# Kernel optimization log

Measured on AMD Instinct MI355X. Metric: run time of the kernel, lower is better.

Reference implementation:

```python
import jax, jax.numpy as jnp
import numpy as np


def setup_inputs() -> dict:
    key = jax.random.key(0)
    kx, kw, kb = jax.random.split(key, 3)
    x = jax.random.normal(kx, (4, 2048, 4096), dtype=jnp.float32)
    weight = jax.random.normal(kw, (4096, 4096), dtype=jnp.float32) * 0.02
    bias = jax.random.normal(kb, (4096,), dtype=jnp.float32) * 0.02
    return {"x": x, "weight": weight, "bias": bias}


def _binarize_except_outliers(w):
    # Outlier mask from global weight stats (computed from w itself; in torch it
    # is cached after the first call but the values are identical every step).
    mean = jnp.mean(w)
    std = jnp.std(w, ddof=1)  # torch.std default is the unbiased estimator
    lower = mean - 1.96 * std
    upper = mean + 1.96 * std
    outliers = (w < lower) | (w > upper)
    keep = (~outliers).astype(w.dtype)
    # scaling_factor in the torch code: w[~outliers].abs().mean(-1) on the
    # flattened masked-select -> a single SCALAR, detached from the graph.
    scale = jax.lax.stop_gradient(jnp.sum(jnp.abs(w) * keep) / jnp.sum(keep))
    # NOTE: the torch code assigns STE-sign values and then immediately
    # overwrites them with w * scale, so the effective math is:
    w_bin = jnp.where(outliers, w, w * scale)
    return w_bin


def reference(x, weight, bias):
    w_bin = _binarize_except_outliers(weight)  # [out, in]
    # F.linear(x, w, b) = x @ w.T + b
    return jnp.einsum("bsi,oi->bso", x, w_bin) + bias
```

## Files before the change

kernel.cpp:

```cpp
#include <hip/hip_runtime.h>
#include <hip/hip_bf16.h>
#include <math.h>

#define MDIM 8192
#define NDIM 4096
#define KDIM 4096
#define WELEMS 16777216
#define XELEMS 33554432

typedef __attribute__((ext_vector_type(8))) short bf16x8;
typedef __attribute__((ext_vector_type(4))) float f32x4;

__device__ __forceinline__ unsigned short f2bf(float f) {
  unsigned int u = __float_as_uint(f);
  u += 0x7fffu + ((u >> 16) & 1u);
  return (unsigned short)(u >> 16);
}

__device__ __forceinline__ void gload16(const void* g, void* l) {
  __builtin_amdgcn_global_load_lds(
      (const __attribute__((address_space(1))) void*)g,
      (__attribute__((address_space(3))) void*)l, 16, 0, 0);
}

template <int MODE>
__global__ __launch_bounds__(256)
void np_stage1(const float* __restrict__ w, float* __restrict__ C,
               float* __restrict__ C2, const float* __restrict__ scal) {
  __shared__ float ls[32], ls2[32];
  const int t = threadIdx.x;
  const int leaf = t >> 3, j = t & 7;
  const size_t base = (size_t)blockIdx.x * 4096 + leaf * 128 + j;
  float mean = 0.f, lower = 0.f, upper = 0.f;
  if (MODE == 1) mean = scal[0];
  if (MODE == 2) { lower = scal[1]; upper = scal[2]; }
  float r = 0.f, r2 = 0.f;
#pragma unroll
  for (int s = 0; s < 16; s++) {
    float v = w[base + s * 8];
    float tv, tv2 = 0.f;
    if (MODE == 0) tv = v;
    else if (MODE == 1) { float x = v - mean; tv = __fmul_rn(x, x); }
    else {
      bool keep = !(v < lower || v > upper);
      tv = keep ? fabsf(v) : 0.f;
      tv2 = keep ? 1.f : 0.f;
    }
    if (s == 0) { r = tv; r2 = tv2; } else { r += tv; r2 += tv2; }
  }
  r += __shfl_xor(r, 1); r += __shfl_xor(r, 2); r += __shfl_xor(r, 4);
  if (MODE == 2) { r2 += __shfl_xor(r2, 1); r2 += __shfl_xor(r2, 2); r2 += __shfl_xor(r2, 4); }
  if (j == 0) { ls[leaf] = r; if (MODE == 2) ls2[leaf] = r2; }
  __syncthreads();
  if (t == 0) {
    float tmp[32];
    for (int i = 0; i < 32; i++) tmp[i] = ls[i];
    for (int n = 32; n > 1; n >>= 1)
      for (int i = 0; i < n / 2; i++) tmp[i] = tmp[2 * i] + tmp[2 * i + 1];
    C[blockIdx.x] = tmp[0];
    if (MODE == 2) {
      for (int i = 0; i < 32; i++) tmp[i] = ls2[i];
      for (int n = 32; n > 1; n >>= 1)
        for (int i = 0; i < n / 2; i++) tmp[i] = tmp[2 * i] + tmp[2 * i + 1];
      C2[blockIdx.x] = tmp[0];
    }
  }
}

template <int MODE>
__global__ __launch_bounds__(256)
void np_stage2(const float* __restrict__ C, const float* __restrict__ C2,
               float* __restrict__ scal) {
  __shared__ float ls[256], ls2[256];
  const int t = threadIdx.x;
  {
    float v[16];
    for (int i = 0; i < 16; i++) v[i] = C[t * 16 + i];
    for (int n = 16; n > 1; n >>= 1)
      for (int i = 0; i < n / 2; i++) v[i] = v[2 * i] + v[2 * i + 1];
    ls[t] = v[0];
    if (MODE == 2) {
      for (int i = 0; i < 16; i++) v[i] = C2[t * 16 + i];
      for (int n = 16; n > 1; n >>= 1)
        for (int i = 0; i < n / 2; i++) v[i] = v[2 * i] + v[2 * i + 1];
      ls2[t] = v[0];
    }
  }
  __syncthreads();
  if (t == 0) {
    float tmp[256];
    for (int i = 0; i < 256; i++) tmp[i] = ls[i];
    for (int n = 256; n > 1; n >>= 1)
      for (int i = 0; i < n / 2; i++) tmp[i] = tmp[2 * i] + tmp[2 * i + 1];
    float S = tmp[0];
    if (MODE == 0) {
      scal[0] = S / 16777216.0f;
    } else if (MODE == 1) {
      float var = S / 16777215.0f;
      float sd = sqrtf(var);
      float mean = scal[0];
      scal[1] = mean - __fmul_rn(1.96f, sd);
      scal[2] = mean + __fmul_rn(1.96f, sd);
    } else {
      for (int i = 0; i < 256; i++) tmp[i] = ls2[i];
      for (int n = 256; n > 1; n >>= 1)
        for (int i = 0; i < n / 2; i++) tmp[i] = tmp[2 * i] + tmp[2 * i + 1];
      scal[3] = S / tmp[0];
    }
  }
}

__device__ __forceinline__ void pack8(const float* __restrict__ p, unsigned short* dst,
                                      bool dobin, float lower, float upper, float scale) {
  float4 u = *(const float4*)p;
  float4 v = *(const float4*)(p + 4);
  float f[8] = {u.x, u.y, u.z, u.w, v.x, v.y, v.z, v.w};
  unsigned int r[4];
#pragma unroll
  for (int j = 0; j < 4; j++) {
    float a = f[2 * j], b = f[2 * j + 1];
    if (dobin) {
      bool oa = (a < lower) || (a > upper);
      bool ob = (b < lower) || (b > upper);
      a = oa ? a : __fmul_rn(a, scale);
      b = ob ? b : __fmul_rn(b, scale);
    }
    r[j] = (unsigned int)f2bf(a) | ((unsigned int)f2bf(b) << 16);
  }
  *(uint4*)dst = make_uint4(r[0], r[1], r[2], r[3]);
}

__global__ __launch_bounds__(256)
void convert_w(const float* __restrict__ w, unsigned short* __restrict__ wb,
               const float* __restrict__ scal) {
  float lower = scal[1], upper = scal[2], scale = scal[3];
  int tid = blockIdx.x * blockDim.x + threadIdx.x;
  int nth = gridDim.x * blockDim.x;
  int nc = WELEMS / 8;
  for (int i = tid; i < nc; i += nth)
    pack8(w + (size_t)i * 8, wb + (size_t)i * 8, true, lower, upper, scale);
}

__global__ __launch_bounds__(256)
void convert_x(const float* __restrict__ x, unsigned short* __restrict__ xb) {
  int tid = blockIdx.x * blockDim.x + threadIdx.x;
  int nth = gridDim.x * blockDim.x;
  int nc = XELEMS / 8;
  for (int i = tid; i < nc; i += nth)
    pack8(x + (size_t)i * 8, xb + (size_t)i * 8, false, 0.f, 0.f, 0.f);
}


#define VM2  asm volatile("s_waitcnt vmcnt(2)" ::: "memory")
#define VM0  asm volatile("s_waitcnt vmcnt(0)" ::: "memory")
#define LGK8 asm volatile("s_waitcnt lgkmcnt(8)" ::: "memory")
#define PSYNC { asm volatile("" ::: "memory"); __builtin_amdgcn_s_barrier(); asm volatile("" ::: "memory"); }

#define LDA(buf, mh) { \
  a[0][0] = *(const bf16x8*)&sA[buf][wm][((mh)*64 +  0 + fr)*64 + koo0]; \
  a[0][1] = *(const bf16x8*)&sA[buf][wm][((mh)*64 +  0 + fr)*64 + koo1]; \
  a[1][0] = *(const bf16x8*)&sA[buf][wm][((mh)*64 + 16 + fr)*64 + koo0]; \
  a[1][1] = *(const bf16x8*)&sA[buf][wm][((mh)*64 + 16 + fr)*64 + koo1]; \
  a[2][0] = *(const bf16x8*)&sA[buf][wm][((mh)*64 + 32 + fr)*64 + koo0]; \
  a[2][1] = *(const bf16x8*)&sA[buf][wm][((mh)*64 + 32 + fr)*64 + koo1]; \
  a[3][0] = *(const bf16x8*)&sA[buf][wm][((mh)*64 + 48 + fr)*64 + koo0]; \
  a[3][1] = *(const bf16x8*)&sA[buf][wm][((mh)*64 + 48 + fr)*64 + koo1]; }

#define LDB(buf, nh) { \
  b[0][0] = *(const bf16x8*)&sB[buf][wnh][(wnq*64 + (nh)*32 +  0 + fr)*64 + koo0]; \
  b[0][1] = *(const bf16x8*)&sB[buf][wnh][(wnq*64 + (nh)*32 +  0 + fr)*64 + koo1]; \
  b[1][0] = *(const bf16x8*)&sB[buf][wnh][(wnq*64 + (nh)*32 + 16 + fr)*64 + koo0]; \
  b[1][1] = *(const bf16x8*)&sB[buf][wnh][(wnq*64 + (nh)*32 + 16 + fr)*64 + koo1]; }

#define MM1(m, n, ks) acc[m][n] = __builtin_amdgcn_mfma_f32_16x16x32_bf16(a[(m)&3][ks], b[(n)&1][ks], acc[m][n], 0, 0, 0)
#define MMKS(mh, nh, ks) { \
  MM1((mh)*4+0, (nh)*2+0, ks); MM1((mh)*4+0, (nh)*2+1, ks); \
  MM1((mh)*4+1, (nh)*2+0, ks); MM1((mh)*4+1, (nh)*2+1, ks); \
  MM1((mh)*4+2, (nh)*2+0, ks); MM1((mh)*4+2, (nh)*2+1, ks); \
  MM1((mh)*4+3, (nh)*2+0, ks); MM1((mh)*4+3, (nh)*2+1, ks); }
#define MM(mh, nh) { \
  __builtin_amdgcn_s_setprio(1); \
  MMKS(mh, nh, 0); MMKS(mh, nh, 1); \
  __builtin_amdgcn_s_setprio(0); }

#define STGA(buf, q, ku) { \
  gload16(xbp + aoff[0][q] + (ku), &sA[buf][0][(q)*4096 + t8]); \
  gload16(xbp + aoff[1][q] + (ku), &sA[buf][1][(q)*4096 + t8]); }
#define STGB(buf, h, ku) { \
  gload16(wbp + boff[h][0] + (ku), &sB[buf][h][t8]); \
  gload16(wbp + boff[h][1] + (ku), &sB[buf][h][4096 + t8]); }

__global__ __launch_bounds__(512, 2)
void gemm256(const unsigned short* __restrict__ xbp, const unsigned short* __restrict__ wbp,
             const float* __restrict__ bias, float* __restrict__ out) {
  __shared__ unsigned short sA[2][2][8192];
  __shared__ unsigned short sB[2][2][8192];

  const int bid = blockIdx.x;
  const int swz = (bid & 7) * 64 + (bid >> 3);
  const int bm = swz >> 4;
  const int bn = swz & 15;

  const int t = threadIdx.x;
  const int lane = t & 63;
  const int wid = t >> 6;
  const int wm = wid >> 2;
  const int wn = wid & 3;
  const int wnh = wn >> 1;
  const int wnq = wn & 1;
  const int fr = lane & 15;
  const int ko = (lane >> 4) * 8;
  const int xr = (fr & 7) << 3;
  const int koo0 = ko ^ xr;
  const int koo1 = (32 + ko) ^ xr;

  const int t8 = t * 8;
  const int rl = t >> 3;
  const int cs = ((t & 7) * 8) ^ ((rl & 7) << 3);
  size_t aoff[2][2], boff[2][2];
#pragma unroll
  for (int h = 0; h < 2; h++)
#pragma unroll
    for (int q = 0; q < 2; q++) {
      aoff[h][q] = (size_t)(bm * 256 + h * 128 + q * 64 + rl) * KDIM + cs;
      boff[h][q] = (size_t)(bn * 256 + h * 128 + q * 64 + rl) * KDIM + cs;
    }

  f32x4 acc[8][4];
#pragma unroll
  for (int i = 0; i < 8; i++)
#pragma unroll
    for (int j = 0; j < 4; j++) acc[i][j] = {0.f, 0.f, 0.f, 0.f};

  bf16x8 a[4][2], b[2][2];

  STGA(0, 0, 0); STGA(0, 1, 0); STGB(0, 0, 0); STGB(0, 1, 0);
  STGA(1, 0, 64);
  VM2; PSYNC;

  const int NIT = KDIM / 128;
  for (int it = 0; it < NIT; ++it) {
    const bool last = (it == NIT - 1);
    const int kuB = it * 128 + 64;
    const int kuN = kuB + 64;

    LDA(0, 0); LDB(0, 0);
    STGA(1, 1, kuB);
    LGK8; PSYNC;
    MM(0, 0); PSYNC;

    LDB(0, 1);
    STGB(1, 0, kuB);
    PSYNC;
    MM(0, 1); PSYNC;

    LDA(0, 1);
    STGB(1, 1, kuB);
    PSYNC;
    MM(1, 1); PSYNC;

    LDB(0, 0);
    if (!last) STGA(0, 0, kuN);
    if (last) { VM0; } else { VM2; }
    PSYNC;
    MM(1, 0); PSYNC;

    LDA(1, 0); LDB(1, 0);
    if (!last) STGA(0, 1, kuN);
    LGK8; PSYNC;
    MM(0, 0); PSYNC;

    LDB(1, 1);
    if (!last) STGB(0, 0, kuN);
    PSYNC;
    MM(0, 1); PSYNC;

    LDA(1, 1);
    if (!last) STGB(0, 1, kuN);
    PSYNC;
    MM(1, 1); PSYNC;

    LDB(1, 0);
    if (!last) {
      STGA(1, 0, kuN + 64);
      VM2;
    }
    PSYNC;
    MM(1, 0); PSYNC;
  }

#pragma unroll
  for (int nn = 0; nn < 4; ++nn) {
    const int col = bn * 256 + wn * 64 + nn * 16 + (lane & 15);
    const float bv = bias[col];
#pragma unroll
    for (int m = 0; m < 8; ++m) {
      const int row0 = bm * 256 + wm * 128 + m * 16 + (lane >> 4) * 4;
#pragma unroll
      for (int q = 0; q < 4; ++q)
        out[(size_t)(row0 + q) * NDIM + col] = acc[m][nn][q] + bv;
    }
  }
}

template <bool A_BF16, bool B_BF16>
__global__ __launch_bounds__(256)
void gemm_bt(const void* __restrict__ Av, const void* __restrict__ Bv,
             const float* __restrict__ bias, float* __restrict__ out,
             const float* __restrict__ scal) {
  __shared__ unsigned short sAt[2][128 * 32];
  __shared__ unsigned short sBt[2][128 * 32];
  float lower = 0.f, upper = 0.f, scale = 0.f;
  if constexpr (!B_BF16) { lower = scal[1]; upper = scal[2]; scale = scal[3]; }
  const unsigned short* Ab = (const unsigned short*)Av;
  const float* Af = (const float*)Av;
  const unsigned short* Bb = (const unsigned short*)Bv;
  const float* Bf = (const float*)Bv;
  int bid = blockIdx.x;
  int swz = (bid & 7) * 256 + (bid >> 3);
  int bm = swz >> 5, bn = swz & 31;
  const int t = threadIdx.x, lane = t & 63, wid = t >> 6;
  const int wm = wid >> 1, wn = wid & 1;
  const int e0 = t * 8, e1 = e0 + 2048;
  const size_t aOff0 = (size_t)(bm * 128 + (e0 >> 5)) * KDIM + (e0 & 31);
  const size_t aOff1 = (size_t)(bm * 128 + (e1 >> 5)) * KDIM + (e1 & 31);
  const size_t bOff0 = (size_t)(bn * 128 + (e0 >> 5)) * KDIM + (e0 & 31);
  const size_t bOff1 = (size_t)(bn * 128 + (e1 >> 5)) * KDIM + (e1 & 31);
  f32x4 acc[4][4];
#pragma unroll
  for (int i = 0; i < 4; i++)
#pragma unroll
    for (int j = 0; j < 4; j++) acc[i][j] = {0.f, 0.f, 0.f, 0.f};
  auto stage = [&](int buf, int k0) {
    if constexpr (A_BF16) {
      gload16(Ab + aOff0 + k0, &sAt[buf][e0]);
      gload16(Ab + aOff1 + k0, &sAt[buf][e1]);
    } else {
      pack8(Af + aOff0 + k0, &sAt[buf][e0], false, 0.f, 0.f, 0.f);
      pack8(Af + aOff1 + k0, &sAt[buf][e1], false, 0.f, 0.f, 0.f);
    }
    if constexpr (B_BF16) {
      gload16(Bb + bOff0 + k0, &sBt[buf][e0]);
      gload16(Bb + bOff1 + k0, &sBt[buf][e1]);
    } else {
      pack8(Bf + bOff0 + k0, &sBt[buf][e0], true, lower, upper, scale);
      pack8(Bf + bOff1 + k0, &sBt[buf][e1], true, lower, upper, scale);
    }
  };
  stage(0, 0);
  const int NT = KDIM / 32;
  const int ko = (lane >> 4) * 8, fr = lane & 15;
  for (int tt = 0; tt < NT; ++tt) {
    int cur = tt & 1;
    __syncthreads();
    if (tt + 1 < NT) stage(cur ^ 1, (tt + 1) * 32);
    bf16x8 a[4], b[4];
#pragma unroll
    for (int i = 0; i < 4; i++) {
      a[i] = *(const bf16x8*)&sAt[cur][(wm * 64 + i * 16 + fr) * 32 + ko];
      b[i] = *(const bf16x8*)&sBt[cur][(wn * 64 + i * 16 + fr) * 32 + ko];
    }
#pragma unroll
    for (int i = 0; i < 4; i++)
#pragma unroll
      for (int j = 0; j < 4; j++)
        acc[i][j] = __builtin_amdgcn_mfma_f32_16x16x32_bf16(a[i], b[j], acc[i][j], 0, 0, 0);
  }
  const int colbase = bn * 128 + wn * 64 + (lane & 15);
  const int rowbase = bm * 128 + wm * 64 + (lane >> 4) * 4;
#pragma unroll
  for (int j = 0; j < 4; j++) {
    int col = colbase + j * 16;
    float bv = bias[col];
#pragma unroll
    for (int i = 0; i < 4; i++) {
      int row0 = rowbase + i * 16;
#pragma unroll
      for (int q = 0; q < 4; q++)
        out[(size_t)(row0 + q) * NDIM + col] = acc[i][j][q] + bv;
    }
  }
}

extern "C" void kernel_launch(void* const* d_in, const int* in_sizes, int n_in,
                              void* d_out, int out_size, void* d_ws, size_t ws_size,
                              hipStream_t stream) {
  const float* x = (const float*)d_in[0];
  const float* w = (const float*)d_in[1];
  const float* bias = (const float*)d_in[2];
  float* out = (float*)d_out;
  char* ws = (char*)d_ws;

  const size_t xb_b = (size_t)XELEMS * 2;
  const size_t wb_b = (size_t)WELEMS * 2;
  const size_t c_b = 4 * 4096 * sizeof(float);
  const bool full = ws_size >= xb_b + wb_b + c_b + 64;
  const bool wonly = !full && ws_size >= wb_b + c_b + 64;

  unsigned short *xb = nullptr, *wb = nullptr;
  float *C1, *scal;
  if (full) {
    xb = (unsigned short*)ws;
    wb = (unsigned short*)(ws + xb_b);
    C1 = (float*)(ws + xb_b + wb_b);
  } else if (wonly) {
    wb = (unsigned short*)ws;
    C1 = (float*)(ws + wb_b);
  } else {
    C1 = (float*)ws;
  }
  float* C2 = C1 + 4096;
  float* C3 = C2 + 4096;
  float* C4 = C3 + 4096;
  scal = C4 + 4096;

  np_stage1<0><<<dim3(4096), dim3(256), 0, stream>>>(w, C1, nullptr, scal);
  np_stage2<0><<<dim3(1), dim3(256), 0, stream>>>(C1, nullptr, scal);
  np_stage1<1><<<dim3(4096), dim3(256), 0, stream>>>(w, C2, nullptr, scal);
  np_stage2<1><<<dim3(1), dim3(256), 0, stream>>>(C2, nullptr, scal);
  np_stage1<2><<<dim3(4096), dim3(256), 0, stream>>>(w, C3, C4, scal);
  np_stage2<2><<<dim3(1), dim3(256), 0, stream>>>(C3, C4, scal);

  if (full) {
    convert_w<<<dim3(2048), dim3(256), 0, stream>>>(w, wb, scal);
    convert_x<<<dim3(4096), dim3(256), 0, stream>>>(x, xb);
    gemm256<<<dim3(512), dim3(512), 0, stream>>>(xb, wb, bias, out);
  } else if (wonly) {
    convert_w<<<dim3(2048), dim3(256), 0, stream>>>(w, wb, scal);
    gemm_bt<false, true><<<dim3(2048), dim3(256), 0, stream>>>(x, wb, bias, out, scal);
  } else {
    gemm_bt<false, false><<<dim3(2048), dim3(256), 0, stream>>>(x, w, bias, out, scal);
  }
}
```

Baseline: 431.5 us.

## Keep both B fragment halves in registers and prefetch B tiles earlier

Splits the B register fragments into two sets (b0/b1) so the fourth MFMA phase reuses b0 instead of reloading it from LDS, removing one LDS read batch per half-iteration. The global-to-LDS schedule is reordered so B tiles for the next K-step are issued earlier, in larger groups, with the wait threshold raised from vmcnt(2) to vmcnt(6). This deepens prefetch of W relative to X. The cost is more VGPRs and possible hazards if the reordered loads overwrite LDS buffers still being read.

```diff
diff --git a/kernel.cpp b/kernel.cpp
--- a/kernel.cpp
+++ b/kernel.cpp
@@ -151,7 +151,7 @@
 }
 
 
-#define VM2  asm volatile("s_waitcnt vmcnt(2)" ::: "memory")
+#define VM6  asm volatile("s_waitcnt vmcnt(6)" ::: "memory")
 #define VM0  asm volatile("s_waitcnt vmcnt(0)" ::: "memory")
 #define LGK8 asm volatile("s_waitcnt lgkmcnt(8)" ::: "memory")
 #define PSYNC { asm volatile("" ::: "memory"); __builtin_amdgcn_s_barrier(); asm volatile("" ::: "memory"); }
@@ -166,21 +166,21 @@
   a[3][0] = *(const bf16x8*)&sA[buf][wm][((mh)*64 + 48 + fr)*64 + koo0]; \
   a[3][1] = *(const bf16x8*)&sA[buf][wm][((mh)*64 + 48 + fr)*64 + koo1]; }
 
-#define LDB(buf, nh) { \
-  b[0][0] = *(const bf16x8*)&sB[buf][wnh][(wnq*64 + (nh)*32 +  0 + fr)*64 + koo0]; \
-  b[0][1] = *(const bf16x8*)&sB[buf][wnh][(wnq*64 + (nh)*32 +  0 + fr)*64 + koo1]; \
-  b[1][0] = *(const bf16x8*)&sB[buf][wnh][(wnq*64 + (nh)*32 + 16 + fr)*64 + koo0]; \
-  b[1][1] = *(const bf16x8*)&sB[buf][wnh][(wnq*64 + (nh)*32 + 16 + fr)*64 + koo1]; }
-
-#define MM1(m, n, ks) acc[m][n] = __builtin_amdgcn_mfma_f32_16x16x32_bf16(a[(m)&3][ks], b[(n)&1][ks], acc[m][n], 0, 0, 0)
-#define MMKS(mh, nh, ks) { \
-  MM1((mh)*4+0, (nh)*2+0, ks); MM1((mh)*4+0, (nh)*2+1, ks); \
-  MM1((mh)*4+1, (nh)*2+0, ks); MM1((mh)*4+1, (nh)*2+1, ks); \
-  MM1((mh)*4+2, (nh)*2+0, ks); MM1((mh)*4+2, (nh)*2+1, ks); \
-  MM1((mh)*4+3, (nh)*2+0, ks); MM1((mh)*4+3, (nh)*2+1, ks); }
-#define MM(mh, nh) { \
+#define LDBX(buf, nh, bb) { \
+  bb[0][0] = *(const bf16x8*)&sB[buf][wnh][(wnq*64 + (nh)*32 +  0 + fr)*64 + koo0]; \
+  bb[0][1] = *(const bf16x8*)&sB[buf][wnh][(wnq*64 + (nh)*32 +  0 + fr)*64 + koo1]; \
+  bb[1][0] = *(const bf16x8*)&sB[buf][wnh][(wnq*64 + (nh)*32 + 16 + fr)*64 + koo0]; \
+  bb[1][1] = *(const bf16x8*)&sB[buf][wnh][(wnq*64 + (nh)*32 + 16 + fr)*64 + koo1]; }
+
+#define MM1(m, n, ks, bb) acc[m][n] = __builtin_amdgcn_mfma_f32_16x16x32_bf16(a[(m)&3][ks], bb[(n)&1][ks], acc[m][n], 0, 0, 0)
+#define MMKS(mh, nh, ks, bb) { \
+  MM1((mh)*4+0, (nh)*2+0, ks, bb); MM1((mh)*4+0, (nh)*2+1, ks, bb); \
+  MM1((mh)*4+1, (nh)*2+0, ks, bb); MM1((mh)*4+1, (nh)*2+1, ks, bb); \
+  MM1((mh)*4+2, (nh)*2+0, ks, bb); MM1((mh)*4+2, (nh)*2+1, ks, bb); \
+  MM1((mh)*4+3, (nh)*2+0, ks, bb); MM1((mh)*4+3, (nh)*2+1, ks, bb); }
+#define MM(mh, nh, bb) { \
   __builtin_amdgcn_s_setprio(1); \
-  MMKS(mh, nh, 0); MMKS(mh, nh, 1); \
+  MMKS(mh, nh, 0, bb); MMKS(mh, nh, 1, bb); \
   __builtin_amdgcn_s_setprio(0); }
 
 #define STGA(buf, q, ku) { \
@@ -232,61 +232,55 @@
 #pragma unroll
     for (int j = 0; j < 4; j++) acc[i][j] = {0.f, 0.f, 0.f, 0.f};
 
-  bf16x8 a[4][2], b[2][2];
-
-  STGA(0, 0, 0); STGA(0, 1, 0); STGB(0, 0, 0); STGB(0, 1, 0);
-  STGA(1, 0, 64);
-  VM2; PSYNC;
+  bf16x8 a[4][2], b0[2][2], b1[2][2];
+
+  STGB(0, 0, 0); STGB(0, 1, 0); STGA(0, 0, 0); STGA(0, 1, 0);
+  STGB(1, 0, 64); STGB(1, 1, 64); STGA(1, 0, 64);
+  VM6; PSYNC;
 
   const int NIT = KDIM / 128;
   for (int it = 0; it < NIT; ++it) {
     const bool last = (it == NIT - 1);
     const int kuB = it * 128 + 64;
     const int kuN = kuB + 64;
-
-    LDA(0, 0); LDB(0, 0);
+    const int kuL = kuB + 128;
+
+    LDA(0, 0); LDBX(0, 0, b0);
     STGA(1, 1, kuB);
     LGK8; PSYNC;
-    MM(0, 0); PSYNC;
-
-    LDB(0, 1);
-    STGB(1, 0, kuB);
-    PSYNC;
-    MM(0, 1); PSYNC;
+    MM(0, 0, b0); PSYNC;
+
+    LDBX(0, 1, b1);
+    PSYNC;
+    MM(0, 1, b1); PSYNC;
 
     LDA(0, 1);
-    STGB(1, 1, kuB);
-    PSYNC;
-    MM(1, 1); PSYNC;
-
-    LDB(0, 0);
+    if (!last) { STGB(0, 0, kuN); STGB(0, 1, kuN); }
+    PSYNC;
+    MM(1, 1, b1); PSYNC;
+
     if (!last) STGA(0, 0, kuN);
-    if (last) { VM0; } else { VM2; }
-    PSYNC;
-    MM(1, 0); PSYNC;
-
-    LDA(1, 0); LDB(1, 0);
+    if (last) { VM0; } else { VM6; }
+    PSYNC;
+    MM(1, 0, b0); PSYNC;
+
+    LDA(1, 0); LDBX(1, 0, b0);
     if (!last) STGA(0, 1, kuN);
     LGK8; PSYNC;
-    MM(0, 0); PSYNC;
-
-    LDB(1, 1);
-    if (!last) STGB(0, 0, kuN);
-    PSYNC;
-    MM(0, 1); PSYNC;
+    MM(0, 0, b0); PSYNC;
+
+    LDBX(1, 1, b1);
+    PSYNC;
+    MM(0, 1, b1); PSYNC;
 
     LDA(1, 1);
-    if (!last) STGB(0, 1, kuN);
-    PSYNC;
-    MM(1, 1); PSYNC;
-
-    LDB(1, 0);
-    if (!last) {
-      STGA(1, 0, kuN + 64);
-      VM2;
-    }
-    PSYNC;
-    MM(1, 0); PSYNC;
+    if (!last) { STGB(1, 0, kuL); STGB(1, 1, kuL); }
+    PSYNC;
+    MM(1, 1, b1); PSYNC;
+
+    if (!last) { STGA(1, 0, kuL); VM6; }
+    PSYNC;
+    MM(1, 0, b0); PSYNC;
   }
 
 #pragma unroll
```

Result: faster. 414.3 us (-4.0%).
